# Kernel tuning notes

Measured on AMD Instinct MI355X. Metric: run time of the kernel, lower is better.

The kernel has to match this reference:

```python
import math
import jax, jax.numpy as jnp
import numpy as np

NUM_HEADS = 8


def _bl(x, w):
    # x: [B, ..., D], w: [B, O, D] -> [B, ..., O]
    return jnp.einsum('b...d,bod->b...o', x, w)


def setup_inputs() -> dict:
    key = jax.random.key(0)
    ks = jax.random.split(key, 5)
    B, C, P, D = 4, 16, 512, 256
    return {
        'qz': jax.random.normal(ks[0], (B, C, P, D), dtype=jnp.float32),
        'time_u': jax.random.normal(ks[1], (B, D, D), dtype=jnp.float32),
        'time_v': jax.random.normal(ks[2], (B, D, D), dtype=jnp.float32),
        'channel_u': jax.random.normal(ks[3], (B, D, D), dtype=jnp.float32),
        'channel_v': jax.random.normal(ks[4], (B, D, D), dtype=jnp.float32),
    }


def _time_msg(qz, u, v, num_heads):
    B, C, P, D = qz.shape
    H = num_heads
    R = D // H
    qu = _bl(qz, u).reshape(B, C, P, H, R).transpose(0, 1, 3, 2, 4)  # bchpr
    qv = _bl(qz, v).reshape(B, C, P, H, R).transpose(0, 1, 3, 2, 4)  # bchqr
    attn = jnp.einsum('bchpr,bchqr->bchpq', qu, qv) / math.sqrt(R)
    attn = jax.nn.softmax(attn, axis=-1)
    msg = jnp.einsum('bchpq,bcqd->bchpd', attn, qz)
    return msg.mean(axis=2)  # [B, C, P, D]


def _chan_msg(qz, u, v, num_heads):
    B, C, P, D = qz.shape
    H = num_heads
    R = D // H
    qu = _bl(qz, u).reshape(B, C, P, H, R).transpose(0, 2, 3, 1, 4)  # bphcr
    qv = _bl(qz, v).reshape(B, C, P, H, R).transpose(0, 2, 3, 1, 4)  # bphfr
    attn = jnp.einsum('bphcr,bphfr->bphcf', qu, qv) / math.sqrt(R)
    attn = jax.nn.softmax(attn, axis=-1)
    qzp = qz.transpose(0, 2, 1, 3)  # [B, P, C, D]
    msg = jnp.einsum('bphcf,bpfd->bphcd', attn, qzp).mean(axis=2)  # [B, P, C, D]
    return msg.transpose(0, 2, 1, 3)  # [B, C, P, D]


def reference(qz, time_u, time_v, channel_u, channel_v):
    m_t = _time_msg(qz, time_u, time_v, NUM_HEADS)
    m_c = _chan_msg(qz, channel_u, channel_v, NUM_HEADS)
    return (m_t, m_c)
```

## Files before the change

kernel.cpp:

```cpp
#include <hip/hip_runtime.h>
#include <hip/hip_bf16.h>
#include <stdint.h>

#define B_ 4
#define C_ 16
#define P_ 512
#define D_ 256
#define H_ 8
#define SCALE 0.17677669529663687f
#define NE 8388608

typedef float4 f4;
typedef uint32_t u32;
typedef __attribute__((ext_vector_type(4))) float f32x4;
typedef __attribute__((ext_vector_type(8))) short short8;

__device__ __forceinline__ unsigned short bf16bits(float x) {
  union { __hip_bfloat16 h; unsigned short u; } cv;
  cv.h = __float2bfloat16(x);
  return cv.u;
}
__device__ __forceinline__ float bf2f(unsigned short u) {
  return __uint_as_float((u32)u << 16);
}
__device__ __forceinline__ u32 packbf2(float a, float b) {
  return ((u32)bf16bits(b) << 16) | bf16bits(a);
}

__global__ __launch_bounds__(256)
void prep_qz(const float* __restrict__ qz, ushort* __restrict__ qzh,
             ushort* __restrict__ qzl, ushort* __restrict__ qzT) {
  const int bc = blockIdx.y;
  const int pt = blockIdx.x >> 2, dt = blockIdx.x & 3;
  const int t = threadIdx.x;
  const int row = t >> 2, cq = t & 3;
  __shared__ float T[64][65];

  const int p = pt * 64 + row;
  const int d0 = dt * 64 + cq * 16;
  const size_t base = (size_t)bc * 131072 + (size_t)p * 256 + d0;
  float v[16];
#pragma unroll
  for (int i = 0; i < 4; ++i) {
    f4 x = *(const f4*)(qz + base + i * 4);
    v[i*4+0] = x.x; v[i*4+1] = x.y; v[i*4+2] = x.z; v[i*4+3] = x.w;
  }
  ushort hs[16], ls[16];
#pragma unroll
  for (int e = 0; e < 16; ++e) {
    unsigned short hb = bf16bits(v[e]);
    hs[e] = hb;
    ls[e] = bf16bits(v[e] - bf2f(hb));
    T[cq * 16 + e][row] = v[e];
  }
  *(ushort4*)(qzh + base)     = make_ushort4(hs[0],hs[1],hs[2],hs[3]);
  *(ushort4*)(qzh + base + 4) = make_ushort4(hs[4],hs[5],hs[6],hs[7]);
  *(ushort4*)(qzh + base + 8) = make_ushort4(hs[8],hs[9],hs[10],hs[11]);
  *(ushort4*)(qzh + base +12) = make_ushort4(hs[12],hs[13],hs[14],hs[15]);
  *(ushort4*)(qzl + base)     = make_ushort4(ls[0],ls[1],ls[2],ls[3]);
  *(ushort4*)(qzl + base + 4) = make_ushort4(ls[4],ls[5],ls[6],ls[7]);
  *(ushort4*)(qzl + base + 8) = make_ushort4(ls[8],ls[9],ls[10],ls[11]);
  *(ushort4*)(qzl + base +12) = make_ushort4(ls[12],ls[13],ls[14],ls[15]);
  __syncthreads();
  const int drow = t >> 2, pq = t & 3;
  ushort os[16];
#pragma unroll
  for (int e = 0; e < 16; ++e) os[e] = bf16bits(T[drow][pq * 16 + e]);
  const size_t tbase = (size_t)bc * 131072 + (size_t)(dt * 64 + drow) * 512 + pt * 64 + pq * 16;
  *(ushort4*)(qzT + tbase)     = make_ushort4(os[0],os[1],os[2],os[3]);
  *(ushort4*)(qzT + tbase + 4) = make_ushort4(os[4],os[5],os[6],os[7]);
  *(ushort4*)(qzT + tbase + 8) = make_ushort4(os[8],os[9],os[10],os[11]);
  *(ushort4*)(qzT + tbase +12) = make_ushort4(os[12],os[13],os[14],os[15]);
}

__global__ __launch_bounds__(256)
void prep_w(const float* __restrict__ tu, const float* __restrict__ tv,
            const float* __restrict__ cu, const float* __restrict__ cv,
            ushort* __restrict__ wh, ushort* __restrict__ wl) {
  const int e4 = blockIdx.x * 256 + threadIdx.x;
  const int idx = e4 * 4;
  const int k0 = idx & 255;
  const int n  = (idx >> 8) & 511;
  const int b  = (idx >> 17) & 3;
  const int br = idx >> 19;
  const float* src;
  float sc;
  if (br == 0) {
    if (n < 256) { src = tu + ((size_t)b * 256 + n) * 256 + k0; sc = SCALE; }
    else         { src = tv + ((size_t)b * 256 + (n - 256)) * 256 + k0; sc = 1.f; }
  } else {
    if (n < 256) { src = cu + ((size_t)b * 256 + n) * 256 + k0; sc = SCALE; }
    else         { src = cv + ((size_t)b * 256 + (n - 256)) * 256 + k0; sc = 1.f; }
  }
  f4 x = *(const f4*)src;
  float v[4] = {x.x * sc, x.y * sc, x.z * sc, x.w * sc};
  ushort hs[4], ls[4];
#pragma unroll
  for (int e = 0; e < 4; ++e) {
    unsigned short hb = bf16bits(v[e]);
    hs[e] = hb;
    ls[e] = bf16bits(v[e] - bf2f(hb));
  }
  const size_t dst = ((size_t)(br * 4 + b) * 512 + n) * 256 + k0;
  *(ushort4*)(wh + dst) = make_ushort4(hs[0], hs[1], hs[2], hs[3]);
  *(ushort4*)(wl + dst) = make_ushort4(ls[0], ls[1], ls[2], ls[3]);
}

__global__ __launch_bounds__(256, 2)
void proj_all(const ushort* __restrict__ qzh, const ushort* __restrict__ qzl,
              const ushort* __restrict__ wh, const ushort* __restrict__ wl,
              ushort* __restrict__ quh, ushort* __restrict__ qul,
              ushort* __restrict__ qvh, ushort* __restrict__ qvl,
              float* __restrict__ qcu, float* __restrict__ qcv) {
  __shared__ char smem[65536];
  const int b = blockIdx.z;
  const int m0 = blockIdx.y * 128;
  const int nt = blockIdx.x;
  const int br = nt >> 2;
  const int n0l = (nt & 3) * 128;
  const int tid = threadIdx.x;
  const int w = tid >> 6, lane = tid & 63;
  const int g = lane >> 4, li = lane & 15;
  const int wm = w >> 1, wn = w & 1;

  f32x4 acc[4][4];
#pragma unroll
  for (int i = 0; i < 4; ++i)
#pragma unroll
    for (int j = 0; j < 4; ++j) acc[i][j] = f32x4{0.f,0.f,0.f,0.f};

  auto stage = [&](int buf, int ks) {
#pragma unroll
    for (int i = 0; i < 4; ++i) {
      int cch = i * 256 + tid;
      int row = cch >> 3, col = cch & 7;
      const ushort* s = (col < 4 ? qzh : qzl) + (size_t)(b * 8192 + m0 + row) * 256 + ks * 32 + (col & 3) * 8;
      uint4 v = *(const uint4*)s;
      *(uint4*)(smem + buf * 16384 + row * 128 + ((col * 16) ^ ((row & 7) << 4))) = v;
    }
#pragma unroll
    for (int i = 0; i < 4; ++i) {
      int cch = i * 256 + tid;
      int row = cch >> 3, col = cch & 7;
      const ushort* s = (col < 4 ? wh : wl) + ((size_t)(br * 4 + b) * 512 + n0l + row) * 256 + ks * 32 + (col & 3) * 8;
      uint4 v = *(const uint4*)s;
      *(uint4*)(smem + 32768 + buf * 16384 + row * 128 + ((col * 16) ^ ((row & 7) << 4))) = v;
    }
  };

  stage(0, 0);
  __syncthreads();
  int buf = 0;
  for (int ks = 0; ks < 8; ++ks) {
    if (ks < 7) stage(buf ^ 1, ks + 1);
    const char* Ab = smem + buf * 16384;
    const char* Bb = smem + 32768 + buf * 16384;
    const int sw = (li & 7) << 4;
    short8 ah[4], al[4];
#pragma unroll
    for (int mt = 0; mt < 4; ++mt) {
      int r = (wm * 64 + mt * 16 + li) * 128;
      ah[mt] = *(const short8*)(Ab + r + ((g * 16) ^ sw));
      al[mt] = *(const short8*)(Ab + r + ((64 + g * 16) ^ sw));
    }
#pragma unroll
    for (int nt2 = 0; nt2 < 4; ++nt2) {
      int r = (wn * 64 + nt2 * 16 + li) * 128;
      short8 bh = *(const short8*)(Bb + r + ((g * 16) ^ sw));
      short8 bl = *(const short8*)(Bb + r + ((64 + g * 16) ^ sw));
#pragma unroll
      for (int mt = 0; mt < 4; ++mt) {
        acc[mt][nt2] = __builtin_amdgcn_mfma_f32_16x16x32_bf16(ah[mt], bh, acc[mt][nt2], 0, 0, 0);
        acc[mt][nt2] = __builtin_amdgcn_mfma_f32_16x16x32_bf16(ah[mt], bl, acc[mt][nt2], 0, 0, 0);
        acc[mt][nt2] = __builtin_amdgcn_mfma_f32_16x16x32_bf16(al[mt], bh, acc[mt][nt2], 0, 0, 0);
      }
    }
    __syncthreads();
    buf ^= 1;
  }

#pragma unroll
  for (int mt = 0; mt < 4; ++mt) {
#pragma unroll
    for (int nt2 = 0; nt2 < 4; ++nt2) {
      int nG = n0l + wn * 64 + nt2 * 16 + li;
#pragma unroll
      for (int j = 0; j < 4; ++j) {
        int m = m0 + wm * 64 + mt * 16 + g * 4 + j;
        int cc = m >> 9, p = m & 511;
        float val = acc[mt][nt2][j];
        if (br == 0) {
          int nn = nG & 255;
          int h = nn >> 5, r = nn & 31;
          size_t dst = ((((size_t)b * 16 + cc) * 8 + h) * 512 + p) * 32 + r;
          unsigned short hb = bf16bits(val);
          unsigned short lb = bf16bits(val - bf2f(hb));
          if (nG < 256) { quh[dst] = hb; qul[dst] = lb; }
          else          { qvh[dst] = hb; qvl[dst] = lb; }
        } else {
          size_t dst = ((size_t)(b * 16 + cc) * 512 + p) * 256 + (nG & 255);
          if (nG < 256) qcu[dst] = val;
          else          qcv[dst] = val;
        }
      }
    }
  }
}

__global__ __launch_bounds__(256, 2)
void time_attn_v2(const ushort* __restrict__ quh, const ushort* __restrict__ qul,
                  const ushort* __restrict__ qvh, const ushort* __restrict__ qvl,
                  const ushort* __restrict__ qzT, float* __restrict__ out) {
  __shared__ char lds[65536];
  const int p0 = blockIdx.x * 64;
  const int bc = blockIdx.z * 16 + blockIdx.y;
  const int tid = threadIdx.x;
  const int w = tid >> 6, lane = tid & 63;
  const int g = lane >> 4, li = lane & 15;
  const int sw = (li & 7) << 4;

  f32x4 macc[32];
#pragma unroll
  for (int kt = 0; kt < 32; ++kt) macc[kt] = f32x4{0.f,0.f,0.f,0.f};

  for (int h = 0; h < H_; ++h) {
    __syncthreads();
    const size_t hb = (size_t)bc * 131072 + h * 16384;
    const ushort* qvhH = qvh + hb;
    const ushort* qvlH = qvl + hb;
#pragma unroll
    for (int i = 0; i < 16; ++i) {
      int cch = i * 256 + tid;
      int key = cch >> 3, col = cch & 7;
      const ushort* s = (col < 4 ? qvhH : qvlH) + key * 32 + (col & 3) * 8;
      uint4 v = *(const uint4*)s;
      *(uint4*)(lds + key * 128 + ((col * 16) ^ ((key & 7) << 4))) = v;
    }
    const size_t qoff = hb + (size_t)(p0 + w * 16 + li) * 32 + g * 8;
    short8 bh = *(const short8*)(quh + qoff);
    short8 bl = *(const short8*)(qul + qoff);
    __syncthreads();

    float m = -3.402823e38f, l = 0.f;
#pragma unroll 4
    for (int kt = 0; kt < 32; ++kt) {
      const char* rp = lds + (kt * 16 + li) * 128;
      short8 a_h = *(const short8*)(rp + ((g * 16) ^ sw));
      short8 a_l = *(const short8*)(rp + ((64 + g * 16) ^ sw));
      f32x4 t = f32x4{0.f,0.f,0.f,0.f};
      t = __builtin_amdgcn_mfma_f32_16x16x32_bf16(a_h, bh, t, 0, 0, 0);
      t = __builtin_amdgcn_mfma_f32_16x16x32_bf16(a_h, bl, t, 0, 0, 0);
      t = __builtin_amdgcn_mfma_f32_16x16x32_bf16(a_l, bh, t, 0, 0, 0);
      float tm = fmaxf(fmaxf(t[0], t[1]), fmaxf(t[2], t[3]));
      tm = fmaxf(tm, __shfl_xor(tm, 16));
      tm = fmaxf(tm, __shfl_xor(tm, 32));
      float mn = fmaxf(m, tm);
      float ts = __expf(t[0] - mn) + __expf(t[1] - mn) + __expf(t[2] - mn) + __expf(t[3] - mn);
      ts += __shfl_xor(ts, 16);
      ts += __shfl_xor(ts, 32);
      l = l * __expf(m - mn) + ts;
      m = mn;
    }
    float rinv = 0.125f / l;
#pragma unroll
    for (int kt = 0; kt < 32; ++kt) {
      const char* rp = lds + (kt * 16 + li) * 128;
      short8 a_h = *(const short8*)(rp + ((g * 16) ^ sw));
      short8 a_l = *(const short8*)(rp + ((64 + g * 16) ^ sw));
      f32x4 t = f32x4{0.f,0.f,0.f,0.f};
      t = __builtin_amdgcn_mfma_f32_16x16x32_bf16(a_h, bh, t, 0, 0, 0);
      t = __builtin_amdgcn_mfma_f32_16x16x32_bf16(a_h, bl, t, 0, 0, 0);
      t = __builtin_amdgcn_mfma_f32_16x16x32_bf16(a_l, bh, t, 0, 0, 0);
#pragma unroll
      for (int j = 0; j < 4; ++j)
        macc[kt][j] += __expf(t[j] - m) * rinv;
    }
  }

  __syncthreads();
  {
    const int q_l = w * 16 + li;
#pragma unroll
    for (int kt = 0; kt < 32; ++kt) {
      u32 u0 = packbf2(macc[kt][0], macc[kt][1]);
      u32 u1 = packbf2(macc[kt][2], macc[kt][3]);
      *(uint2*)(lds + q_l * 1024 + ((kt * 32 + g * 8) ^ sw)) = make_uint2(u0, u1);
    }
  }
  __syncthreads();

  f32x4 oacc[16];
#pragma unroll
  for (int dt = 0; dt < 16; ++dt) oacc[dt] = f32x4{0.f,0.f,0.f,0.f};
  const ushort* qzTb = qzT + (size_t)bc * 131072;
#pragma unroll 2
  for (int ks = 0; ks < 16; ++ks) {
    short8 pa = *(const short8*)(lds + (w * 16 + li) * 1024 + ((ks * 64 + g * 16) ^ sw));
#pragma unroll
    for (int dt = 0; dt < 16; ++dt) {
      short8 bz = *(const short8*)(qzTb + (size_t)(dt * 16 + li) * 512 + ks * 32 + g * 8);
      oacc[dt] = __builtin_amdgcn_mfma_f32_16x16x32_bf16(pa, bz, oacc[dt], 0, 0, 0);
    }
  }
  float* outB = out + (size_t)bc * 131072;
#pragma unroll
  for (int dt = 0; dt < 16; ++dt)
#pragma unroll
    for (int j = 0; j < 4; ++j)
      outB[(size_t)(p0 + w * 16 + g * 4 + j) * 256 + dt * 16 + li] = oacc[dt][j];
}

__global__ __launch_bounds__(64)
void chan_attn_kernel(const float* __restrict__ qu, const float* __restrict__ qv,
                      const float* __restrict__ qz, float* __restrict__ out) {
  const int p = blockIdx.x, b = blockIdx.y;
  __shared__ float buf0[16][260];
  __shared__ float qvC[16][260];
  __shared__ float A_m[16][17];

  const int tid = threadIdx.x;
  const int f = tid & 15;
  const int gg = tid >> 4;

#pragma unroll
  for (int cc = 0; cc < 16; ++cc) {
    size_t off = (((size_t)b * C_ + cc) * P_ + p) * D_ + tid*4;
    *(f4*)&buf0[cc][tid*4] = *(const f4*)&qu[off];
    *(f4*)&qvC[cc][tid*4]  = *(const f4*)&qv[off];
  }
  __syncthreads();

  float am[4] = {0.f, 0.f, 0.f, 0.f};
  for (int h = 0; h < H_; ++h) {
    f4 vr[8];
#pragma unroll
    for (int i = 0; i < 8; ++i) vr[i] = *(const f4*)&qvC[f][h*32 + i*4];
    float sj[4];
#pragma unroll
    for (int j = 0; j < 4; ++j) {
      int cc = gg + 4*j;
      float ssum = 0.f;
#pragma unroll
      for (int i = 0; i < 8; ++i) {
        f4 uu = *(const f4*)&buf0[cc][h*32 + i*4];
        ssum += uu.x*vr[i].x + uu.y*vr[i].y + uu.z*vr[i].z + uu.w*vr[i].w;
      }
      sj[j] = ssum;
    }
#pragma unroll
    for (int j = 0; j < 4; ++j) {
      float mx = sj[j];
      for (int off = 8; off >= 1; off >>= 1) mx = fmaxf(mx, __shfl_xor(mx, off));
      float pv = __expf(sj[j] - mx);
      float sum = pv;
      for (int off = 8; off >= 1; off >>= 1) sum += __shfl_xor(sum, off);
      am[j] += pv * (0.125f / sum);
    }
  }
#pragma unroll
  for (int j = 0; j < 4; ++j) A_m[gg + 4*j][f] = am[j];
  __syncthreads();
#pragma unroll
  for (int cc = 0; cc < 16; ++cc) {
    size_t off = (((size_t)b * C_ + cc) * P_ + p) * D_ + tid*4;
    *(f4*)&buf0[cc][tid*4] = *(const f4*)&qz[off];
  }
  __syncthreads();

  f4 acc4[16];
#pragma unroll
  for (int cc = 0; cc < 16; ++cc) acc4[cc] = make_float4(0.f, 0.f, 0.f, 0.f);
#pragma unroll
  for (int ff = 0; ff < 16; ++ff) {
    f4 z = *(const f4*)&buf0[ff][tid*4];
#pragma unroll
    for (int cc = 0; cc < 16; ++cc) {
      float aa = A_m[cc][ff];
      acc4[cc].x = fmaf(aa, z.x, acc4[cc].x);
      acc4[cc].y = fmaf(aa, z.y, acc4[cc].y);
      acc4[cc].z = fmaf(aa, z.z, acc4[cc].z);
      acc4[cc].w = fmaf(aa, z.w, acc4[cc].w);
    }
  }
#pragma unroll
  for (int cc = 0; cc < 16; ++cc) {
    size_t off = (((size_t)b * C_ + cc) * P_ + p) * D_ + tid*4;
    *(f4*)&out[off] = acc4[cc];
  }
}

extern "C" void kernel_launch(void* const* d_in, const int* in_sizes, int n_in,
                              void* d_out, int out_size, void* d_ws, size_t ws_size,
                              hipStream_t stream) {
  const float* qz = (const float*)d_in[0];
  const float* tu = (const float*)d_in[1];
  const float* tv = (const float*)d_in[2];
  const float* cu = (const float*)d_in[3];
  const float* cv = (const float*)d_in[4];
  float* out_mt = (float*)d_out;
  float* out_mc = out_mt + (size_t)NE;

  ushort* W = (ushort*)d_ws;
  ushort* qzh = W;
  ushort* qzl = qzh + NE;
  ushort* qzT = qzl + NE;
  ushort* wh  = qzT + NE;
  ushort* wl  = wh + 1048576;
  ushort* quh = wl + 1048576;
  ushort* qul = quh + NE;
  ushort* qvh = qul + NE;
  ushort* qvl = qvh + NE;
  float* qcu = out_mt;
  float* qcv = out_mc;

  hipLaunchKernelGGL(prep_qz, dim3(32, 64), dim3(256), 0, stream, qz, qzh, qzl, qzT);
  hipLaunchKernelGGL(prep_w, dim3(1024), dim3(256), 0, stream, tu, tv, cu, cv, wh, wl);
  hipLaunchKernelGGL(proj_all, dim3(8, 64, 4), dim3(256), 0, stream,
                     qzh, qzl, wh, wl, quh, qul, qvh, qvl, qcu, qcv);
  hipLaunchKernelGGL(chan_attn_kernel, dim3(P_, B_), dim3(64), 0, stream,
                     qcu, qcv, qz, out_mc);
  hipLaunchKernelGGL(time_attn_v2, dim3(8, 16, 4), dim3(256), 0, stream,
                     quh, qul, qvh, qvl, qzT, out_mt);
}
```

Before: 301.0 us.

## Compute time-attention scores once per head in registers, dropping recompute and LDS staging

The time attention kernel used to compute QK scores twice per head, once for an online max/sum pass and once for the weighted accumulation. It now computes all 32 score tiles once, holds them in registers, and runs an exact max and sum before normalizing. Keys are read straight from global memory instead of being staged through swizzled LDS with barriers. The head-summed probability accumulator is stored as packed bf16 to cut register use. Keeping 128 score floats live adds register pressure, and rounding the accumulator to bf16 after each head adds error.

```diff
diff --git a/kernel.cpp b/kernel.cpp
--- a/kernel.cpp
+++ b/kernel.cpp
@@ -23,6 +23,8 @@
 __device__ __forceinline__ float bf2f(unsigned short u) {
   return __uint_as_float((u32)u << 16);
 }
+__device__ __forceinline__ float bf2f_lo(u32 a) { return __uint_as_float(a << 16); }
+__device__ __forceinline__ float bf2f_hi(u32 a) { return __uint_as_float(a & 0xffff0000u); }
 __device__ __forceinline__ u32 packbf2(float a, float b) {
   return ((u32)bf16bits(b) << 16) | bf16bits(a);
 }
@@ -208,7 +210,7 @@
 }
 
 __global__ __launch_bounds__(256, 2)
-void time_attn_v2(const ushort* __restrict__ quh, const ushort* __restrict__ qul,
+void time_attn_v3(const ushort* __restrict__ quh, const ushort* __restrict__ qul,
                   const ushort* __restrict__ qvh, const ushort* __restrict__ qvl,
                   const ushort* __restrict__ qzT, float* __restrict__ out) {
   __shared__ char lds[65536];
@@ -219,73 +221,81 @@
   const int g = lane >> 4, li = lane & 15;
   const int sw = (li & 7) << 4;
 
-  f32x4 macc[32];
-#pragma unroll
-  for (int kt = 0; kt < 32; ++kt) macc[kt] = f32x4{0.f,0.f,0.f,0.f};
+  u32 macc_p[64];
+#pragma unroll
+  for (int i = 0; i < 64; ++i) macc_p[i] = 0u;
 
   for (int h = 0; h < H_; ++h) {
-    __syncthreads();
     const size_t hb = (size_t)bc * 131072 + h * 16384;
-    const ushort* qvhH = qvh + hb;
-    const ushort* qvlH = qvl + hb;
-#pragma unroll
-    for (int i = 0; i < 16; ++i) {
-      int cch = i * 256 + tid;
-      int key = cch >> 3, col = cch & 7;
-      const ushort* s = (col < 4 ? qvhH : qvlH) + key * 32 + (col & 3) * 8;
-      uint4 v = *(const uint4*)s;
-      *(uint4*)(lds + key * 128 + ((col * 16) ^ ((key & 7) << 4))) = v;
-    }
     const size_t qoff = hb + (size_t)(p0 + w * 16 + li) * 32 + g * 8;
     short8 bh = *(const short8*)(quh + qoff);
     short8 bl = *(const short8*)(qul + qoff);
-    __syncthreads();
-
-    float m = -3.402823e38f, l = 0.f;
-#pragma unroll 4
+
+    const ushort* kh = qvh + hb + (size_t)li * 32 + g * 8;
+    const ushort* kl = qvl + hb + (size_t)li * 32 + g * 8;
+
+    f32x4 t[32];
+#pragma unroll
     for (int kt = 0; kt < 32; ++kt) {
-      const char* rp = lds + (kt * 16 + li) * 128;
-      short8 a_h = *(const short8*)(rp + ((g * 16) ^ sw));
-      short8 a_l = *(const short8*)(rp + ((64 + g * 16) ^ sw));
-      f32x4 t = f32x4{0.f,0.f,0.f,0.f};
-      t = __builtin_amdgcn_mfma_f32_16x16x32_bf16(a_h, bh, t, 0, 0, 0);
-      t = __builtin_amdgcn_mfma_f32_16x16x32_bf16(a_h, bl, t, 0, 0, 0);
-      t = __builtin_amdgcn_mfma_f32_16x16x32_bf16(a_l, bh, t, 0, 0, 0);
-      float tm = fmaxf(fmaxf(t[0], t[1]), fmaxf(t[2], t[3]));
-      tm = fmaxf(tm, __shfl_xor(tm, 16));
-      tm = fmaxf(tm, __shfl_xor(tm, 32));
-      float mn = fmaxf(m, tm);
-      float ts = __expf(t[0] - mn) + __expf(t[1] - mn) + __expf(t[2] - mn) + __expf(t[3] - mn);
-      ts += __shfl_xor(ts, 16);
-      ts += __shfl_xor(ts, 32);
-      l = l * __expf(m - mn) + ts;
-      m = mn;
-    }
+      short8 a_h = *(const short8*)(kh + kt * 512);
+      short8 a_l = *(const short8*)(kl + kt * 512);
+      f32x4 acc = f32x4{0.f,0.f,0.f,0.f};
+      acc = __builtin_amdgcn_mfma_f32_16x16x32_bf16(a_h, bh, acc, 0, 0, 0);
+      acc = __builtin_amdgcn_mfma_f32_16x16x32_bf16(a_h, bl, acc, 0, 0, 0);
+      acc = __builtin_amdgcn_mfma_f32_16x16x32_bf16(a_l, bh, acc, 0, 0, 0);
+      t[kt] = acc;
+    }
+
+    float m4[8];
+#pragma unroll
+    for (int o = 0; o < 8; ++o) {
+      float a0 = fmaxf(fmaxf(t[o*4+0][0], t[o*4+0][1]), fmaxf(t[o*4+0][2], t[o*4+0][3]));
+      float a1 = fmaxf(fmaxf(t[o*4+1][0], t[o*4+1][1]), fmaxf(t[o*4+1][2], t[o*4+1][3]));
+      float a2 = fmaxf(fmaxf(t[o*4+2][0], t[o*4+2][1]), fmaxf(t[o*4+2][2], t[o*4+2][3]));
+      float a3 = fmaxf(fmaxf(t[o*4+3][0], t[o*4+3][1]), fmaxf(t[o*4+3][2], t[o*4+3][3]));
+      m4[o] = fmaxf(fmaxf(a0, a1), fmaxf(a2, a3));
+    }
+    float m = fmaxf(fmaxf(fmaxf(m4[0], m4[1]), fmaxf(m4[2], m4[3])),
+                    fmaxf(fmaxf(m4[4], m4[5]), fmaxf(m4[6], m4[7])));
+    m = fmaxf(m, __shfl_xor(m, 16));
+    m = fmaxf(m, __shfl_xor(m, 32));
+
+    float s4[32];
+#pragma unroll
+    for (int kt = 0; kt < 32; ++kt) {
+      float p0v = __expf(t[kt][0] - m);
+      float p1v = __expf(t[kt][1] - m);
+      float p2v = __expf(t[kt][2] - m);
+      float p3v = __expf(t[kt][3] - m);
+      t[kt][0] = p0v; t[kt][1] = p1v; t[kt][2] = p2v; t[kt][3] = p3v;
+      s4[kt] = (p0v + p1v) + (p2v + p3v);
+    }
+    float s8[8];
+#pragma unroll
+    for (int o = 0; o < 8; ++o)
+      s8[o] = (s4[o*4+0] + s4[o*4+1]) + (s4[o*4+2] + s4[o*4+3]);
+    float l = ((s8[0] + s8[1]) + (s8[2] + s8[3])) + ((s8[4] + s8[5]) + (s8[6] + s8[7]));
+    l += __shfl_xor(l, 16);
+    l += __shfl_xor(l, 32);
     float rinv = 0.125f / l;
+
 #pragma unroll
     for (int kt = 0; kt < 32; ++kt) {
-      const char* rp = lds + (kt * 16 + li) * 128;
-      short8 a_h = *(const short8*)(rp + ((g * 16) ^ sw));
-      short8 a_l = *(const short8*)(rp + ((64 + g * 16) ^ sw));
-      f32x4 t = f32x4{0.f,0.f,0.f,0.f};
-      t = __builtin_amdgcn_mfma_f32_16x16x32_bf16(a_h, bh, t, 0, 0, 0);
-      t = __builtin_amdgcn_mfma_f32_16x16x32_bf16(a_h, bl, t, 0, 0, 0);
-      t = __builtin_amdgcn_mfma_f32_16x16x32_bf16(a_l, bh, t, 0, 0, 0);
-#pragma unroll
-      for (int j = 0; j < 4; ++j)
-        macc[kt][j] += __expf(t[j] - m) * rinv;
-    }
-  }
-
-  __syncthreads();
+      u32 a0 = macc_p[kt*2], a1 = macc_p[kt*2+1];
+      float v0 = fmaf(t[kt][0], rinv, bf2f_lo(a0));
+      float v1 = fmaf(t[kt][1], rinv, bf2f_hi(a0));
+      float v2 = fmaf(t[kt][2], rinv, bf2f_lo(a1));
+      float v3 = fmaf(t[kt][3], rinv, bf2f_hi(a1));
+      macc_p[kt*2]   = packbf2(v0, v1);
+      macc_p[kt*2+1] = packbf2(v2, v3);
+    }
+  }
+
   {
     const int q_l = w * 16 + li;
 #pragma unroll
-    for (int kt = 0; kt < 32; ++kt) {
-      u32 u0 = packbf2(macc[kt][0], macc[kt][1]);
-      u32 u1 = packbf2(macc[kt][2], macc[kt][3]);
-      *(uint2*)(lds + q_l * 1024 + ((kt * 32 + g * 8) ^ sw)) = make_uint2(u0, u1);
-    }
+    for (int kt = 0; kt < 32; ++kt)
+      *(uint2*)(lds + q_l * 1024 + ((kt * 32 + g * 8) ^ sw)) = make_uint2(macc_p[kt*2], macc_p[kt*2+1]);
   }
   __syncthreads();
 
@@ -419,6 +429,6 @@
                      qzh, qzl, wh, wl, quh, qul, qvh, qvl, qcu, qcv);
   hipLaunchKernelGGL(chan_attn_kernel, dim3(P_, B_), dim3(64), 0, stream,
                      qcu, qcv, qz, out_mc);
-  hipLaunchKernelGGL(time_attn_v2, dim3(8, 16, 4), dim3(256), 0, stream,
+  hipLaunchKernelGGL(time_attn_v3, dim3(8, 16, 4), dim3(256), 0, stream,
                      quh, qul, qvh, qvl, qzT, out_mt);
 }
```

After: 321.7 us. 1.07x slower.
